# Kernel tuning notes

Hardware: AMD Instinct MI355X
Metric: run time of the kernel (lower is better)

## Reference

```python
import jax, jax.numpy as jnp
import numpy as np
from jax import lax

B, T, E, K = 64, 512, 2048, 32


def setup_inputs() -> dict:
    key = jax.random.key(0)
    ks = jax.random.split(key, 8)
    X = jax.random.normal(ks[0], (B, T, E), dtype=jnp.float32)
    y = jax.random.randint(ks[1], (B, T), 0, K, dtype=jnp.int32)
    # variable-length mask: lengths in [T//2, T], position 0 always valid
    lengths = jax.random.randint(ks[2], (B,), T // 2, T + 1)
    mask = (jnp.arange(T)[None, :] < lengths[:, None])
    W = jax.random.normal(ks[3], (E, K), dtype=jnp.float32) * 0.02
    b = jnp.zeros((K,), dtype=jnp.float32)
    transitions = jax.random.normal(ks[4], (K, K), dtype=jnp.float32) * 0.1
    start_transitions = jax.random.normal(ks[5], (K,), dtype=jnp.float32) * 0.1
    end_transitions = jax.random.normal(ks[6], (K,), dtype=jnp.float32) * 0.1
    return {"X": X, "y": y, "mask": mask, "W": W, "b": b,
            "transitions": transitions,
            "start_transitions": start_transitions,
            "end_transitions": end_transitions}


def _input_likelihood(logits, mask, trans, start, end):
    # forward algorithm (log partition), AllenNLP semantics
    lt = jnp.transpose(logits, (1, 0, 2))  # [T,B,K]
    mt = mask.T                            # [T,B]
    alpha0 = start[None, :] + lt[0]        # [B,K]

    def step(alpha, xm):
        x, m = xm  # x:[B,K], m:[B]
        inner = alpha[:, :, None] + trans[None, :, :] + x[:, None, :]  # [B,K,K]
        new = jax.nn.logsumexp(inner, axis=1)
        return jnp.where(m[:, None], new, alpha), None

    alpha, _ = lax.scan(step, alpha0, (lt[1:], mt[1:]))
    return jax.nn.logsumexp(alpha + end[None, :], axis=1)  # [B]


def _joint_likelihood(logits, tags, mask, trans, start, end):
    maskf = mask.astype(logits.dtype)
    emit = jnp.take_along_axis(logits, tags[:, :, None], axis=2)[:, :, 0]  # [B,T]
    emit_score = jnp.sum(emit * maskf, axis=1)
    trans_sc = trans[tags[:, :-1], tags[:, 1:]]  # [B,T-1]
    trans_score = jnp.sum(trans_sc * maskf[:, 1:], axis=1)
    lengths = jnp.sum(mask.astype(jnp.int32), axis=1)
    last_tags = jnp.take_along_axis(tags, (lengths - 1)[:, None], axis=1)[:, 0]
    return start[tags[:, 0]] + emit_score + trans_score + end[last_tags]


def reference(X, y, mask, W, b, transitions, start_transitions, end_transitions):
    logits = jnp.einsum('bte,ek->btk', X, W) + b  # projection
    log_num = _joint_likelihood(logits, y, mask, transitions,
                                start_transitions, end_transitions)
    log_den = _input_likelihood(logits, mask, transitions,
                                start_transitions, end_transitions)
    # CRF.forward training path: loss = -crf(inputs, tags, mask)
    return -jnp.sum(log_num - log_den)
```

## Files before the change

kernel.cpp:

```cpp
#include <hip/hip_runtime.h>

#define Bn 64
#define Tn 512
#define En 2048
#define Kn 32
#define Mn (Bn*Tn)
#define LOG2E 1.4426950408889634f
#define LN2   0.6931471805599453f

typedef __attribute__((ext_vector_type(8))) short short8;
typedef __attribute__((ext_vector_type(4))) float floatx4;

__device__ inline unsigned int pack_bf16(float a, float b) {
    unsigned int ua = __float_as_uint(a), ub = __float_as_uint(b);
    return ((ua + 0x8000u) >> 16) | (((ub + 0x8000u) & 0xFFFF0000u));
}

__global__ __launch_bounds__(256) void prep_kernel(const float* __restrict__ W,
                                                   unsigned short* __restrict__ Wt,
                                                   float* __restrict__ out) {
    int idx = blockIdx.x * 256 + threadIdx.x;
    int k = idx >> 11, e = idx & 2047;
    float w = W[e * Kn + k];
    Wt[idx] = (unsigned short)((__float_as_uint(w) + 0x8000u) >> 16);
    if (idx == 0) out[0] = 0.f;
}

__global__ __launch_bounds__(256) void gemm_kernel(const float* __restrict__ X,
                                                   const float* __restrict__ bias,
                                                   const unsigned short* __restrict__ Wt,
                                                   float* __restrict__ logits2) {
    __shared__ unsigned short As[64][72];
    __shared__ unsigned short Bs[32][72];

    const int tid  = threadIdx.x;
    const int wave = tid >> 6;
    const int lane = tid & 63;
    const int ml   = lane & 15;
    const int quad = lane >> 4;
    const int row0 = blockIdx.x * 64;

    floatx4 acc0 = {0.f,0.f,0.f,0.f};
    floatx4 acc1 = {0.f,0.f,0.f,0.f};

    for (int ec = 0; ec < En / 64; ++ec) {
        const int e0 = ec * 64;
        float4 xr[4];
        #pragma unroll
        for (int i = 0; i < 4; ++i) {
            int flat = tid + i * 256;
            int r = flat >> 4, q = flat & 15;
            xr[i] = *(const float4*)&X[(size_t)(row0 + r) * En + e0 + q * 4];
        }
        int wrow = tid >> 3, wseg = tid & 7;
        uint4 wr = *(const uint4*)&Wt[wrow * En + e0 + wseg * 8];

        __syncthreads();
        #pragma unroll
        for (int i = 0; i < 4; ++i) {
            int flat = tid + i * 256;
            int r = flat >> 4, q = flat & 15;
            uint2 p; p.x = pack_bf16(xr[i].x, xr[i].y); p.y = pack_bf16(xr[i].z, xr[i].w);
            *(uint2*)&As[r][q * 4] = p;
        }
        *(uint4*)&Bs[wrow][wseg * 8] = wr;
        __syncthreads();

        #pragma unroll
        for (int kk = 0; kk < 2; ++kk) {
            short8 a  = *(const short8*)&As[wave * 16 + ml][kk * 32 + quad * 8];
            short8 b0 = *(const short8*)&Bs[ml][kk * 32 + quad * 8];
            short8 b1 = *(const short8*)&Bs[16 + ml][kk * 32 + quad * 8];
            acc0 = __builtin_amdgcn_mfma_f32_16x16x32_bf16(a, b0, acc0, 0, 0, 0);
            acc1 = __builtin_amdgcn_mfma_f32_16x16x32_bf16(a, b1, acc1, 0, 0, 0);
        }
    }

    const float bc0 = bias[ml], bc1 = bias[16 + ml];
    const int gr = row0 + wave * 16 + quad * 4;
    #pragma unroll
    for (int r = 0; r < 4; ++r) {
        logits2[(size_t)(gr + r) * Kn + ml]      = (acc0[r] + bc0) * LOG2E;
        logits2[(size_t)(gr + r) * Kn + 16 + ml] = (acc1[r] + bc1) * LOG2E;
    }
}

__global__ __launch_bounds__(64) void crf_kernel(const float* __restrict__ logits2,
                                                 const int* __restrict__ y,
                                                 const void* __restrict__ maskp,
                                                 const float* __restrict__ trans,
                                                 const float* __restrict__ start,
                                                 const float* __restrict__ endt,
                                                 float* __restrict__ out) {
    const int b    = blockIdx.x;
    const int lane = threadIdx.x;
    const int j    = lane & 31;
    const int ibase = (lane >> 5) * 16;

    unsigned int first = *(const unsigned int*)maskp;
    int mode;
    if (first <= 1u) mode = 0;
    else if (first == 0x3F800000u) mode = 2;
    else mode = 1;

    int len = 0;
    if (mode == 0) {
        const int* mb = (const int*)maskp + b * Tn;
        for (int t = lane; t < Tn; t += 64) len += (mb[t] != 0);
    } else if (mode == 1) {
        const unsigned char* mb = (const unsigned char*)maskp + b * Tn;
        for (int t = lane; t < Tn; t += 64) len += (mb[t] != 0);
    } else {
        const float* mb = (const float*)maskp + b * Tn;
        for (int t = lane; t < Tn; t += 64) len += (mb[t] != 0.f);
    }
    #pragma unroll
    for (int o = 32; o; o >>= 1) len += __shfl_xor(len, o, 64);

    const int* yb = y + b * Tn;
    float num2 = 0.f;
    for (int t = lane; t < Tn; t += 64) {
        if (t < len) {
            int yt = yb[t];
            num2 += logits2[((size_t)b * Tn + t) * Kn + yt];
            if (t >= 1) num2 += trans[yb[t - 1] * Kn + yt] * LOG2E;
        }
    }
    if (lane == 0) num2 += (start[yb[0]] + endt[yb[len - 1]]) * LOG2E;
    #pragma unroll
    for (int o = 32; o; o >>= 1) num2 += __shfl_xor(num2, o, 64);

    float P[16];
    #pragma unroll
    for (int k = 0; k < 16; ++k)
        P[k] = __builtin_exp2f(trans[(ibase + k) * Kn + j] * LOG2E);

    const float* xrow = logits2 + (size_t)b * Tn * Kn;
    float a = start[j] * LOG2E + xrow[j];
    float S = __shfl(a, 0, 64);
    a -= S;

    float xn = xrow[Kn + j];
    for (int t = 1; t < len; ++t) {
        float xcur = xn;
        int tn = t + 1 < Tn ? t + 1 : Tn - 1;
        xn = xrow[tn * Kn + j];

        float u = __builtin_exp2f(a);
        float w0 = 0.f, w1 = 0.f, w2 = 0.f, w3 = 0.f;
        #pragma unroll
        for (int k = 0; k < 16; k += 4) {
            float u0 = __shfl(u, ibase + k,     64);
            float u1 = __shfl(u, ibase + k + 1, 64);
            float u2 = __shfl(u, ibase + k + 2, 64);
            float u3 = __shfl(u, ibase + k + 3, 64);
            w0 = fmaf(u0, P[k],     w0);
            w1 = fmaf(u1, P[k + 1], w1);
            w2 = fmaf(u2, P[k + 2], w2);
            w3 = fmaf(u3, P[k + 3], w3);
        }
        float w = (w0 + w1) + (w2 + w3);
        w += __shfl_xor(w, 32, 64);
        float n = xcur + __builtin_log2f(w);
        if ((t & 3) == 0) {
            float sg = __shfl(n, 0, 64);
            a = n - sg;
            S += sg;
        } else {
            a = n;
        }
    }

    float v = (lane < 32) ? __builtin_exp2f(a + endt[j] * LOG2E) : 0.f;
    #pragma unroll
    for (int o = 32; o; o >>= 1) v += __shfl_xor(v, o, 64);
    float den2 = S + __builtin_log2f(v);

    if (lane == 0) atomicAdd(out, (den2 - num2) * LN2);
}

extern "C" void kernel_launch(void* const* d_in, const int* in_sizes, int n_in,
                              void* d_out, int out_size, void* d_ws, size_t ws_size,
                              hipStream_t stream) {
    const float* X     = (const float*)d_in[0];
    const int*   y     = (const int*)  d_in[1];
    const void*  mask  =               d_in[2];
    const float* W     = (const float*)d_in[3];
    const float* bias  = (const float*)d_in[4];
    const float* trans = (const float*)d_in[5];
    const float* start = (const float*)d_in[6];
    const float* endt  = (const float*)d_in[7];
    float* out = (float*)d_out;

    float* logits2 = (float*)d_ws;
    unsigned short* Wt = (unsigned short*)((char*)d_ws + (size_t)Mn * Kn * 4);

    prep_kernel<<<256, 256, 0, stream>>>(W, Wt, out);
    gemm_kernel<<<Mn / 64, 256, 0, stream>>>(X, bias, Wt, logits2);
    crf_kernel<<<Bn, 64, 0, stream>>>(logits2, y, mask, trans, start, endt, out);
}
```

Measured before the change: 511.6 us.

## Drop LDS staging in projection GEMM and use readlane broadcast in CRF recurrence

The GEMM now loads X and bf16 W fragments straight from global memory into MFMA operands, removing the shared-memory staging and both block barriers per K-chunk. Each X element is still read once, but W is read by every wave. The CRF forward recursion now has each lane hold all 32 transition columns and broadcasts alpha with scalar readlane instead of cross-half shuffles plus a final xor-shuffle. It also processes timesteps in groups of four with the emission loads prefetched one group ahead. This shortens the serial dependency chain per timestep, at the cost of more registers and duplicated work in the upper half-wave.

```diff
diff --git a/kernel.cpp b/kernel.cpp
--- a/kernel.cpp
+++ b/kernel.cpp
@@ -16,6 +16,10 @@
     return ((ua + 0x8000u) >> 16) | (((ub + 0x8000u) & 0xFFFF0000u));
 }
 
+__device__ inline float rdlane(float v, int l) {
+    return __uint_as_float(__builtin_amdgcn_readlane(__float_as_uint(v), l));
+}
+
 __global__ __launch_bounds__(256) void prep_kernel(const float* __restrict__ W,
                                                    unsigned short* __restrict__ Wt,
                                                    float* __restrict__ out) {
@@ -30,9 +34,6 @@
                                                    const float* __restrict__ bias,
                                                    const unsigned short* __restrict__ Wt,
                                                    float* __restrict__ logits2) {
-    __shared__ unsigned short As[64][72];
-    __shared__ unsigned short Bs[32][72];
-
     const int tid  = threadIdx.x;
     const int wave = tid >> 6;
     const int lane = tid & 63;
@@ -40,40 +41,26 @@
     const int quad = lane >> 4;
     const int row0 = blockIdx.x * 64;
 
+    const float*          xp  = X  + (size_t)(row0 + wave * 16 + ml) * En + quad * 8;
+    const unsigned short* b0p = Wt + ml * En        + quad * 8;
+    const unsigned short* b1p = Wt + (16 + ml) * En + quad * 8;
+
     floatx4 acc0 = {0.f,0.f,0.f,0.f};
     floatx4 acc1 = {0.f,0.f,0.f,0.f};
 
-    for (int ec = 0; ec < En / 64; ++ec) {
-        const int e0 = ec * 64;
-        float4 xr[4];
-        #pragma unroll
-        for (int i = 0; i < 4; ++i) {
-            int flat = tid + i * 256;
-            int r = flat >> 4, q = flat & 15;
-            xr[i] = *(const float4*)&X[(size_t)(row0 + r) * En + e0 + q * 4];
-        }
-        int wrow = tid >> 3, wseg = tid & 7;
-        uint4 wr = *(const uint4*)&Wt[wrow * En + e0 + wseg * 8];
-
-        __syncthreads();
-        #pragma unroll
-        for (int i = 0; i < 4; ++i) {
-            int flat = tid + i * 256;
-            int r = flat >> 4, q = flat & 15;
-            uint2 p; p.x = pack_bf16(xr[i].x, xr[i].y); p.y = pack_bf16(xr[i].z, xr[i].w);
-            *(uint2*)&As[r][q * 4] = p;
-        }
-        *(uint4*)&Bs[wrow][wseg * 8] = wr;
-        __syncthreads();
-
-        #pragma unroll
-        for (int kk = 0; kk < 2; ++kk) {
-            short8 a  = *(const short8*)&As[wave * 16 + ml][kk * 32 + quad * 8];
-            short8 b0 = *(const short8*)&Bs[ml][kk * 32 + quad * 8];
-            short8 b1 = *(const short8*)&Bs[16 + ml][kk * 32 + quad * 8];
-            acc0 = __builtin_amdgcn_mfma_f32_16x16x32_bf16(a, b0, acc0, 0, 0, 0);
-            acc1 = __builtin_amdgcn_mfma_f32_16x16x32_bf16(a, b1, acc1, 0, 0, 0);
-        }
+    #pragma unroll 4
+    for (int e0 = 0; e0 < En; e0 += 32) {
+        float4 xa = *(const float4*)(xp + e0);
+        float4 xb = *(const float4*)(xp + e0 + 4);
+        short8 b0 = *(const short8*)(b0p + e0);
+        short8 b1 = *(const short8*)(b1p + e0);
+        union { unsigned int u[4]; short8 s; } av;
+        av.u[0] = pack_bf16(xa.x, xa.y);
+        av.u[1] = pack_bf16(xa.z, xa.w);
+        av.u[2] = pack_bf16(xb.x, xb.y);
+        av.u[3] = pack_bf16(xb.z, xb.w);
+        acc0 = __builtin_amdgcn_mfma_f32_16x16x32_bf16(av.s, b0, acc0, 0, 0, 0);
+        acc1 = __builtin_amdgcn_mfma_f32_16x16x32_bf16(av.s, b1, acc1, 0, 0, 0);
     }
 
     const float bc0 = bias[ml], bc1 = bias[16 + ml];
@@ -95,7 +82,6 @@
     const int b    = blockIdx.x;
     const int lane = threadIdx.x;
     const int j    = lane & 31;
-    const int ibase = (lane >> 5) * 16;
 
     unsigned int first = *(const unsigned int*)maskp;
     int mode;
@@ -130,45 +116,57 @@
     #pragma unroll
     for (int o = 32; o; o >>= 1) num2 += __shfl_xor(num2, o, 64);
 
-    float P[16];
+    float P[32];
     #pragma unroll
-    for (int k = 0; k < 16; ++k)
-        P[k] = __builtin_exp2f(trans[(ibase + k) * Kn + j] * LOG2E);
+    for (int i = 0; i < 32; ++i)
+        P[i] = __builtin_exp2f(trans[i * Kn + j] * LOG2E);
 
     const float* xrow = logits2 + (size_t)b * Tn * Kn;
     float a = start[j] * LOG2E + xrow[j];
-    float S = __shfl(a, 0, 64);
-    a -= S;
+    float S = 0.f;
 
-    float xn = xrow[Kn + j];
-    for (int t = 1; t < len; ++t) {
-        float xcur = xn;
-        int tn = t + 1 < Tn ? t + 1 : Tn - 1;
-        xn = xrow[tn * Kn + j];
+    float cur[4], nxt[4];
+    #pragma unroll
+    for (int q = 0; q < 4; ++q) {
+        int tq = 1 + q; if (tq > Tn - 1) tq = Tn - 1;
+        cur[q] = xrow[tq * Kn + j];
+    }
 
-        float u = __builtin_exp2f(a);
-        float w0 = 0.f, w1 = 0.f, w2 = 0.f, w3 = 0.f;
+    for (int g = 1; g < len; g += 4) {
         #pragma unroll
-        for (int k = 0; k < 16; k += 4) {
-            float u0 = __shfl(u, ibase + k,     64);
-            float u1 = __shfl(u, ibase + k + 1, 64);
-            float u2 = __shfl(u, ibase + k + 2, 64);
-            float u3 = __shfl(u, ibase + k + 3, 64);
-            w0 = fmaf(u0, P[k],     w0);
-            w1 = fmaf(u1, P[k + 1], w1);
-            w2 = fmaf(u2, P[k + 2], w2);
-            w3 = fmaf(u3, P[k + 3], w3);
+        for (int q = 0; q < 4; ++q) {
+            int tq = g + 4 + q; if (tq > Tn - 1) tq = Tn - 1;
+            nxt[q] = xrow[tq * Kn + j];
         }
-        float w = (w0 + w1) + (w2 + w3);
-        w += __shfl_xor(w, 32, 64);
-        float n = xcur + __builtin_log2f(w);
-        if ((t & 3) == 0) {
-            float sg = __shfl(n, 0, 64);
-            a = n - sg;
-            S += sg;
-        } else {
-            a = n;
+        #pragma unroll
+        for (int q = 0; q < 4; ++q) {
+            if (g + q < len) {
+                float u = __builtin_exp2f(a);
+                float w0 = 0.f, w1 = 0.f, w2 = 0.f, w3 = 0.f;
+                #pragma unroll
+                for (int i = 0; i < 32; i += 4) {
+                    float s0 = rdlane(u, i);
+                    float s1 = rdlane(u, i + 1);
+                    float s2 = rdlane(u, i + 2);
+                    float s3 = rdlane(u, i + 3);
+                    w0 = fmaf(s0, P[i],     w0);
+                    w1 = fmaf(s1, P[i + 1], w1);
+                    w2 = fmaf(s2, P[i + 2], w2);
+                    w3 = fmaf(s3, P[i + 3], w3);
+                }
+                float w = (w0 + w1) + (w2 + w3);
+                float n = cur[q] + __builtin_log2f(w);
+                if (q == 3) {
+                    float sg = rdlane(n, 0);
+                    a = n - sg;
+                    S += sg;
+                } else {
+                    a = n;
+                }
+            }
         }
+        #pragma unroll
+        for (int q = 0; q < 4; ++q) cur[q] = nxt[q];
     }
 
     float v = (lane < 32) ? __builtin_exp2f(a + endt[j] * LOG2E) : 0.f;
```

Result: faster. 466.7 us (-8.8%).
